# Performance work log

Hardware: AMD Instinct MI355X
Metric: run time of the kernel (lower is better)

Reference implementation:

```python
import jax, jax.numpy as jnp
import numpy as np

N = 256       # ImageSize
NC = 8        # coils
NSPOKE = 34   # radial spokes
NVEC = 512    # samples per spoke
M = NSPOKE * NVEC


def setup_inputs() -> dict:
    key = jax.random.key(0)
    k1, k2, k3, k4 = jax.random.split(key, 4)
    X = jax.random.normal(k1, (N, N, 2), dtype=jnp.float32)
    # nonuniform k-space coordinates in [-pi, pi)
    angles = (jax.random.uniform(k2, (M, 2), dtype=jnp.float32) * 2.0 - 1.0) * jnp.pi
    C = jax.random.normal(k3, (NC, N, N, 2), dtype=jnp.float32)   # coil sensitivities (re/im)
    w = jax.random.uniform(k4, (NSPOKE, NVEC), dtype=jnp.float32)  # density compensation
    return {"X": X, "angles": angles, "C": C, "w": w,
            "Nspoke": NSPOKE, "Nvec": NVEC, "Nc": NC}


def _forward(X, angles, C, w, Nspoke, Nvec, Nc):
    # X: (N,N,2) real/imag image; C: (Nc,N,N,2); angles: (M,2); w: (Nspoke,Nvec)
    n = X.shape[0]
    # uniform grid coords; N even -> linspace(-N//2, N//2-1, N) == arange
    x = jnp.arange(-(n // 2), n - (n // 2), dtype=jnp.float32)  # (N,)
    img = (X[..., 0] + 1j * X[..., 1]).astype(jnp.complex64)    # (N,N)
    Cc = (C[..., 0] + 1j * C[..., 1]).astype(jnp.complex64)     # (Nc,N,N)
    src = img[None] * Cc                                        # coil images (Nc,N,N)
    s = angles[:, 0]
    t = angles[:, 1]
    # Type-3 NUFFT as separable direct DFT: y[c,k] = sum_{a,b} src[c,a,b] e^{-i(s_k x_a + t_k x_b)}
    Ea = jnp.exp((-1j) * s[:, None] * x[None, :]).astype(jnp.complex64)  # (M,N)
    Eb = jnp.exp((-1j) * t[:, None] * x[None, :]).astype(jnp.complex64)  # (M,N)
    tmp = jnp.einsum('cab,kb->cka', src, Eb)   # (Nc,M,N) -- dominant intermediate
    y = jnp.einsum('cka,ka->ck', tmp, Ea)      # (Nc,M)
    yc = y.reshape(Nc, Nspoke, Nvec) * w       # density compensation
    y = yc.reshape(Nc, Nspoke * Nvec)
    return jnp.stack([y.real, y.imag], axis=-1)  # (Nc, M, 2) float32


def reference(X, angles, C, w, Nspoke, Nvec, Nc):
    return _forward(X, angles, C, w, Nspoke, Nvec, Nc)
```

## Files before the change

kernel.cpp:

```cpp
#include <hip/hip_runtime.h>

#define NC   8
#define MTOT 17408

typedef __attribute__((ext_vector_type(8)))  short short8;
typedef __attribute__((ext_vector_type(16))) float f32x16;

typedef __attribute__((address_space(3))) unsigned       lds_uint;
typedef const __attribute__((address_space(1))) unsigned glb_uint;

static __device__ __forceinline__ short f2bf(float f) {
    union { float f; unsigned u; } v; v.f = f;
    return (short)((v.u + 0x7fffu + ((v.u >> 16) & 1u)) >> 16);
}

__global__ __launch_bounds__(256) void build_src(
        const float* __restrict__ X, const float* __restrict__ C,
        short* __restrict__ Sr, short* __restrict__ Si) {
    int idx = blockIdx.x * 256 + threadIdx.x;
    int ab = idx & 65535;
    float xr = X[ab * 2 + 0], xi = X[ab * 2 + 1];
    float cr = C[idx * 2 + 0], ci = C[idx * 2 + 1];
    Sr[idx] = f2bf(xr * cr - xi * ci);
    Si[idx] = f2bf(xr * ci + xi * cr);
}

__global__ __launch_bounds__(256) void build_ebt(
        const float* __restrict__ angles, short* __restrict__ EbT) {
    int gid  = blockIdx.x * 256 + threadIdx.x;
    int kt   = gid >> 10;
    int r    = gid & 1023;
    int ks   = r >> 6;
    int lane = r & 63;
    int k    = kt * 32 + (lane & 31);
    float t  = angles[k * 2 + 1];
    short8 re, im;
    #pragma unroll
    for (int j = 0; j < 8; ++j) {
        float xb = (float)(ks * 16 + (lane >> 5) * 8 + j - 128);
        float sn, cs;
        __sincosf(t * xb, &sn, &cs);
        re[j] = f2bf(cs);
        im[j] = f2bf(-sn);
    }
    short* base = EbT + (size_t)(kt * 32 + ks) * 512 + lane * 8;
    *(short8*)(base)        = re;
    *(short8*)(base + 8192) = im;
}

template<int USE_TABLE>
__global__ __launch_bounds__(256, 2) void nufft_fwd(
        const float* __restrict__ angles, const float* __restrict__ w,
        const short* __restrict__ SrP, const short* __restrict__ SiP,
        const short* __restrict__ EbT, float* __restrict__ out) {
    __shared__ char lds[65536];

    const int tid  = threadIdx.x;
    const int lane = tid & 63;
    const int wv   = tid >> 6;
    const int c    = blockIdx.y;
    const int col  = lane & 31;
    const int hi   = lane >> 5;
    const int kt   = blockIdx.x * 4 + wv;
    const int k    = kt * 32 + col;
    const float s  = angles[k * 2 + 0];

    const short* Sr = SrP + c * 65536;
    const short* Si = SiP + c * 65536;

    short8 Br[16], Bi[16];
    if constexpr (USE_TABLE) {
        const short* tb = EbT + (size_t)(kt * 32) * 512 + lane * 8;
        #pragma unroll
        for (int ks = 0; ks < 16; ++ks) {
            Br[ks] = *(const short8*)(tb + ks * 512);
            Bi[ks] = *(const short8*)(tb + 8192 + ks * 512);
        }
    } else {
        const float t = angles[k * 2 + 1];
        #pragma unroll
        for (int ks = 0; ks < 16; ++ks) {
            short8 re, im;
            #pragma unroll
            for (int j = 0; j < 8; ++j) {
                float xb = (float)(ks * 16 + hi * 8 + j - 128);
                float sn, cs;
                __sincosf(t * xb, &sn, &cs);
                re[j] = f2bf(cs);
                im[j] = f2bf(-sn);
            }
            Br[ks] = re; Bi[ks] = im;
        }
    }

    auto stage = [&](int at, int half) {
        #pragma unroll
        for (int it = 0; it < 8; ++it) {
            int L   = it * 256 + tid;
            int row = (L >> 5) & 31;
            int cb  = (L & 31) ^ (row & 7);
            const short* g = ((L >> 10) ? Si : Sr) + (at * 32 + row) * 256 + cb * 8;
            __builtin_amdgcn_global_load_lds(
                (glb_uint*)g,
                (lds_uint*)(lds + half * 32768 + (it * 256 + (tid & ~63)) * 16),
                16, 0, 0);
        }
    };

    float yr = 0.f, yi = 0.f;

    stage(0, 0);
    __syncthreads();

    for (int at = 0; at < 8; ++at) {
        const int cur = at & 1;
        if (at < 7) stage(at + 1, cur ^ 1);

        const char* buf = lds + cur * 32768;
        f32x16 P1 = {0.f}, P2 = {0.f}, P3 = {0.f}, P4 = {0.f};
        const int rowoff = col * 512;
        const int swz    = col & 7;
        #pragma unroll
        for (int ks = 0; ks < 16; ++ks) {
            int slot = ((ks * 2 + hi) ^ swz) << 4;
            short8 Arf = *(const short8*)(buf + rowoff + slot);
            short8 Aif = *(const short8*)(buf + 16384 + rowoff + slot);
            P1 = __builtin_amdgcn_mfma_f32_32x32x16_bf16(Arf, Br[ks], P1, 0, 0, 0);
            P2 = __builtin_amdgcn_mfma_f32_32x32x16_bf16(Aif, Bi[ks], P2, 0, 0, 0);
            P3 = __builtin_amdgcn_mfma_f32_32x32x16_bf16(Arf, Bi[ks], P3, 0, 0, 0);
            P4 = __builtin_amdgcn_mfma_f32_32x32x16_bf16(Aif, Br[ks], P4, 0, 0, 0);
        }
        #pragma unroll
        for (int reg = 0; reg < 16; ++reg) {
            int ap = at * 32 + (reg & 3) + 8 * (reg >> 2) + 4 * hi - 128;
            float Tr = P1[reg] - P2[reg];
            float Ti = P3[reg] + P4[reg];
            float sn, cs;
            __sincosf(s * (float)ap, &sn, &cs);
            yr += cs * Tr + sn * Ti;
            yi += cs * Ti - sn * Tr;
        }
        __syncthreads();
    }

    yr += __shfl_xor(yr, 32);
    yi += __shfl_xor(yi, 32);

    if (hi == 0) {
        float wk = w[k];
        out[((size_t)c * MTOT + k) * 2 + 0] = yr * wk;
        out[((size_t)c * MTOT + k) * 2 + 1] = yi * wk;
    }
}

extern "C" void kernel_launch(void* const* d_in, const int* in_sizes, int n_in,
                              void* d_out, int out_size, void* d_ws, size_t ws_size,
                              hipStream_t stream) {
    const float* X      = (const float*)d_in[0];
    const float* angles = (const float*)d_in[1];
    const float* C      = (const float*)d_in[2];
    const float* w      = (const float*)d_in[3];
    float* out = (float*)d_out;

    short* Sr  = (short*)d_ws;
    short* Si  = Sr + NC * 65536;
    short* EbT = Si + NC * 65536;

    size_t need = ((size_t)NC * 65536 * 2 + (size_t)MTOT * 512) * sizeof(short);
    const bool use_table = ws_size >= need;

    build_src<<<dim3(NC * 65536 / 256), dim3(256), 0, stream>>>(X, C, Sr, Si);

    dim3 grid(MTOT / 128, NC);
    if (use_table) {
        build_ebt<<<dim3(MTOT * 32 / 256), dim3(256), 0, stream>>>(angles, EbT);
        nufft_fwd<1><<<grid, dim3(256), 0, stream>>>(angles, w, Sr, Si, EbT, out);
    } else {
        nufft_fwd<0><<<grid, dim3(256), 0, stream>>>(angles, w, Sr, Si, nullptr, out);
    }
}
```

Measured before the change: 96.52 us.

## Merge prep kernels, single-buffer LDS and stream Eb table to raise occupancy

Fuses the source-building and Eb-table kernels into one launch to save a kernel launch. The main kernel drops its double-buffered LDS (64KB to 32KB) and stops holding the 32-register Eb fragment arrays, instead loading Eb fragments from global memory inside each ks step. Launch bounds go from 2 to 4 blocks per CU, and s_setprio is raised around the MFMA loop. This trades the overlap of the next tile's load with compute, and adds repeated global loads of Eb (8x per tile), in exchange for higher occupancy to hide latency.

```diff
diff --git a/kernel.cpp b/kernel.cpp
--- a/kernel.cpp
+++ b/kernel.cpp
@@ -14,46 +14,48 @@
     return (short)((v.u + 0x7fffu + ((v.u >> 16) & 1u)) >> 16);
 }
 
-__global__ __launch_bounds__(256) void build_src(
+__global__ __launch_bounds__(256) void prep(
         const float* __restrict__ X, const float* __restrict__ C,
-        short* __restrict__ Sr, short* __restrict__ Si) {
-    int idx = blockIdx.x * 256 + threadIdx.x;
-    int ab = idx & 65535;
-    float xr = X[ab * 2 + 0], xi = X[ab * 2 + 1];
-    float cr = C[idx * 2 + 0], ci = C[idx * 2 + 1];
-    Sr[idx] = f2bf(xr * cr - xi * ci);
-    Si[idx] = f2bf(xr * ci + xi * cr);
-}
-
-__global__ __launch_bounds__(256) void build_ebt(
-        const float* __restrict__ angles, short* __restrict__ EbT) {
-    int gid  = blockIdx.x * 256 + threadIdx.x;
-    int kt   = gid >> 10;
-    int r    = gid & 1023;
-    int ks   = r >> 6;
-    int lane = r & 63;
-    int k    = kt * 32 + (lane & 31);
-    float t  = angles[k * 2 + 1];
-    short8 re, im;
-    #pragma unroll
-    for (int j = 0; j < 8; ++j) {
-        float xb = (float)(ks * 16 + (lane >> 5) * 8 + j - 128);
-        float sn, cs;
-        __sincosf(t * xb, &sn, &cs);
-        re[j] = f2bf(cs);
-        im[j] = f2bf(-sn);
+        const float* __restrict__ angles,
+        short* __restrict__ Sr, short* __restrict__ Si,
+        short* __restrict__ EbT) {
+    int bx = blockIdx.x;
+    if (bx < 2048) {
+        int idx = bx * 256 + threadIdx.x;
+        int ab = idx & 65535;
+        float xr = X[ab * 2 + 0], xi = X[ab * 2 + 1];
+        float cr = C[idx * 2 + 0], ci = C[idx * 2 + 1];
+        Sr[idx] = f2bf(xr * cr - xi * ci);
+        Si[idx] = f2bf(xr * ci + xi * cr);
+    } else {
+        int gid  = (bx - 2048) * 256 + threadIdx.x;
+        int kt   = gid >> 10;
+        int r    = gid & 1023;
+        int ks   = r >> 6;
+        int lane = r & 63;
+        int k    = kt * 32 + (lane & 31);
+        float t  = angles[k * 2 + 1];
+        short8 re, im;
+        #pragma unroll
+        for (int j = 0; j < 8; ++j) {
+            float xb = (float)(ks * 16 + (lane >> 5) * 8 + j - 128);
+            float sn, cs;
+            __sincosf(t * xb, &sn, &cs);
+            re[j] = f2bf(cs);
+            im[j] = f2bf(-sn);
+        }
+        short* base = EbT + (size_t)(kt * 32 + ks) * 512 + lane * 8;
+        *(short8*)(base)        = re;
+        *(short8*)(base + 8192) = im;
     }
-    short* base = EbT + (size_t)(kt * 32 + ks) * 512 + lane * 8;
-    *(short8*)(base)        = re;
-    *(short8*)(base + 8192) = im;
 }
 
 template<int USE_TABLE>
-__global__ __launch_bounds__(256, 2) void nufft_fwd(
+__global__ __launch_bounds__(256, 4) void nufft_fwd(
         const float* __restrict__ angles, const float* __restrict__ w,
         const short* __restrict__ SrP, const short* __restrict__ SiP,
         const short* __restrict__ EbT, float* __restrict__ out) {
-    __shared__ char lds[65536];
+    __shared__ char lds[32768];
 
     const int tid  = threadIdx.x;
     const int lane = tid & 63;
@@ -67,33 +69,10 @@
 
     const short* Sr = SrP + c * 65536;
     const short* Si = SiP + c * 65536;
+    const short* tb = EbT + (size_t)(kt * 32) * 512 + lane * 8;
+    const float  t  = USE_TABLE ? 0.f : angles[k * 2 + 1];
 
-    short8 Br[16], Bi[16];
-    if constexpr (USE_TABLE) {
-        const short* tb = EbT + (size_t)(kt * 32) * 512 + lane * 8;
-        #pragma unroll
-        for (int ks = 0; ks < 16; ++ks) {
-            Br[ks] = *(const short8*)(tb + ks * 512);
-            Bi[ks] = *(const short8*)(tb + 8192 + ks * 512);
-        }
-    } else {
-        const float t = angles[k * 2 + 1];
-        #pragma unroll
-        for (int ks = 0; ks < 16; ++ks) {
-            short8 re, im;
-            #pragma unroll
-            for (int j = 0; j < 8; ++j) {
-                float xb = (float)(ks * 16 + hi * 8 + j - 128);
-                float sn, cs;
-                __sincosf(t * xb, &sn, &cs);
-                re[j] = f2bf(cs);
-                im[j] = f2bf(-sn);
-            }
-            Br[ks] = re; Bi[ks] = im;
-        }
-    }
-
-    auto stage = [&](int at, int half) {
+    auto stage = [&](int at) {
         #pragma unroll
         for (int it = 0; it < 8; ++it) {
             int L   = it * 256 + tid;
@@ -102,34 +81,47 @@
             const short* g = ((L >> 10) ? Si : Sr) + (at * 32 + row) * 256 + cb * 8;
             __builtin_amdgcn_global_load_lds(
                 (glb_uint*)g,
-                (lds_uint*)(lds + half * 32768 + (it * 256 + (tid & ~63)) * 16),
+                (lds_uint*)(lds + (it * 256 + (tid & ~63)) * 16),
                 16, 0, 0);
         }
     };
 
     float yr = 0.f, yi = 0.f;
 
-    stage(0, 0);
-    __syncthreads();
+    for (int at = 0; at < 8; ++at) {
+        stage(at);
+        __syncthreads();
 
-    for (int at = 0; at < 8; ++at) {
-        const int cur = at & 1;
-        if (at < 7) stage(at + 1, cur ^ 1);
-
-        const char* buf = lds + cur * 32768;
         f32x16 P1 = {0.f}, P2 = {0.f}, P3 = {0.f}, P4 = {0.f};
         const int rowoff = col * 512;
         const int swz    = col & 7;
+        __builtin_amdgcn_s_setprio(1);
         #pragma unroll
         for (int ks = 0; ks < 16; ++ks) {
+            short8 Brk, Bik;
+            if constexpr (USE_TABLE) {
+                Brk = *(const short8*)(tb + ks * 512);
+                Bik = *(const short8*)(tb + 8192 + ks * 512);
+            } else {
+                #pragma unroll
+                for (int j = 0; j < 8; ++j) {
+                    float xb = (float)(ks * 16 + hi * 8 + j - 128);
+                    float sn, cs;
+                    __sincosf(t * xb, &sn, &cs);
+                    Brk[j] = f2bf(cs);
+                    Bik[j] = f2bf(-sn);
+                }
+            }
             int slot = ((ks * 2 + hi) ^ swz) << 4;
-            short8 Arf = *(const short8*)(buf + rowoff + slot);
-            short8 Aif = *(const short8*)(buf + 16384 + rowoff + slot);
-            P1 = __builtin_amdgcn_mfma_f32_32x32x16_bf16(Arf, Br[ks], P1, 0, 0, 0);
-            P2 = __builtin_amdgcn_mfma_f32_32x32x16_bf16(Aif, Bi[ks], P2, 0, 0, 0);
-            P3 = __builtin_amdgcn_mfma_f32_32x32x16_bf16(Arf, Bi[ks], P3, 0, 0, 0);
-            P4 = __builtin_amdgcn_mfma_f32_32x32x16_bf16(Aif, Br[ks], P4, 0, 0, 0);
+            short8 Arf = *(const short8*)(lds + rowoff + slot);
+            short8 Aif = *(const short8*)(lds + 16384 + rowoff + slot);
+            P1 = __builtin_amdgcn_mfma_f32_32x32x16_bf16(Arf, Brk, P1, 0, 0, 0);
+            P2 = __builtin_amdgcn_mfma_f32_32x32x16_bf16(Aif, Bik, P2, 0, 0, 0);
+            P3 = __builtin_amdgcn_mfma_f32_32x32x16_bf16(Arf, Bik, P3, 0, 0, 0);
+            P4 = __builtin_amdgcn_mfma_f32_32x32x16_bf16(Aif, Brk, P4, 0, 0, 0);
         }
+        __builtin_amdgcn_s_setprio(0);
+
         #pragma unroll
         for (int reg = 0; reg < 16; ++reg) {
             int ap = at * 32 + (reg & 3) + 8 * (reg >> 2) + 4 * hi - 128;
@@ -169,13 +161,13 @@
     size_t need = ((size_t)NC * 65536 * 2 + (size_t)MTOT * 512) * sizeof(short);
     const bool use_table = ws_size >= need;
 
-    build_src<<<dim3(NC * 65536 / 256), dim3(256), 0, stream>>>(X, C, Sr, Si);
-
     dim3 grid(MTOT / 128, NC);
     if (use_table) {
-        build_ebt<<<dim3(MTOT * 32 / 256), dim3(256), 0, stream>>>(angles, EbT);
+        prep<<<dim3(2048 + MTOT * 32 / 256), dim3(256), 0, stream>>>(
+            X, C, angles, Sr, Si, EbT);
         nufft_fwd<1><<<grid, dim3(256), 0, stream>>>(angles, w, Sr, Si, EbT, out);
     } else {
+        prep<<<dim3(2048), dim3(256), 0, stream>>>(X, C, angles, Sr, Si, EbT);
         nufft_fwd<0><<<grid, dim3(256), 0, stream>>>(angles, w, Sr, Si, nullptr, out);
     }
 }
```

Result: slower. 246.6 us (+155.5%).
